# Optimization experiments

Hardware: AMD Instinct MI355X
Metric: run time of the kernel (lower is better)

## Reference

```python
import jax, jax.numpy as jnp
import numpy as np

B, T, C = 8, 512, 512
H, HKV, D = 8, 4, 64
S_MAX = 128
BASE_FREQ = 10000.0
INIT_SIGMA = 256.0
EPS = 1e-6


def _init_positional_kernel(n_heads, head_dim, s_max, base_freq):
    table_size = 2 * s_max + 1
    deltas = jnp.arange(table_size) - s_max
    d_half = head_dim // 2
    freqs = 1.0 / base_freq ** (jnp.arange(d_half, dtype=jnp.float32) / d_half)
    phases = deltas[:, None].astype(jnp.float32) * freqs[None, :]
    P_single = jnp.concatenate([jnp.cos(phases), jnp.sin(phases)], axis=-1)
    return jnp.tile(P_single[None, :, :], (n_heads, 1, 1))


def setup_inputs() -> dict:
    key = jax.random.key(0)
    ks = jax.random.split(key, 6)
    scale = 0.02
    x = jax.random.normal(ks[0], (B, T, C), dtype=jnp.float32)
    Wq = jax.random.normal(ks[1], (C, H * D), dtype=jnp.float32) * scale
    Wk = jax.random.normal(ks[2], (C, HKV * D), dtype=jnp.float32) * scale
    Wv = jax.random.normal(ks[3], (C, HKV * D), dtype=jnp.float32) * scale
    Wproj = jax.random.normal(ks[4], (C, C), dtype=jnp.float32) * scale
    P = _init_positional_kernel(H, D, S_MAX, BASE_FREQ)
    sigma = jnp.full((H,), INIT_SIGMA, dtype=jnp.float32)
    return {"x": x, "Wq": Wq, "Wk": Wk, "Wv": Wv, "Wproj": Wproj, "P": P, "sigma": sigma}


def _norm(t):
    # nGPT-style: unit norm * sqrt(dim)
    dim = t.shape[-1]
    return t * (jnp.sqrt(float(dim)) * jax.lax.rsqrt((t * t).sum(axis=-1, keepdims=True) + EPS))


def _warped_kernel(P, sigma, T_):
    # P: [H, 2*S_MAX+1, D], sigma: [H] -> P_interp: [H, T, T, D]
    positions = jnp.arange(T_)
    delta = positions[:, None] - positions[None, :]  # [T, T]
    s = jnp.abs(sigma) + 1e-6
    delta_warped = S_MAX * jnp.tanh(delta[None, :, :].astype(jnp.float32) / s[:, None, None])
    delta_table = delta_warped + S_MAX  # [H, T, T]
    idx_lo = jnp.floor(delta_table).astype(jnp.int32)
    idx_hi = idx_lo + 1
    frac = delta_table - idx_lo.astype(P.dtype)
    table_max = 2 * S_MAX
    idx_lo = jnp.clip(idx_lo, 0, table_max)
    idx_hi = jnp.clip(idx_hi, 0, table_max)
    head_idx = jnp.arange(H)[:, None, None]
    P_lo = P[head_idx, idx_lo, :]  # [H, T, T, D]
    P_hi = P[head_idx, idx_hi, :]
    return (1 - frac[..., None]) * P_lo + frac[..., None] * P_hi


def reference(x, Wq, Wk, Wv, Wproj, P, sigma):
    q = (x @ Wq).reshape(B, T, H, D)
    k = (x @ Wk).reshape(B, T, HKV, D)
    v = (x @ Wv).reshape(B, T, HKV, D)
    q, k = _norm(q), _norm(k)
    repeats = H // HKV
    k = jnp.repeat(k, repeats, axis=2)
    v = jnp.repeat(v, repeats, axis=2)
    q = q.transpose(0, 2, 1, 3)  # [B, H, T, D]
    k = k.transpose(0, 2, 1, 3)
    v = v.transpose(0, 2, 1, 3)

    sm_scale = 1.0 / jnp.sqrt(float(D))
    P_interp = _warped_kernel(P, sigma, T)  # [H, T, T, D]
    S = jnp.einsum('bhid,hijd,bhjd->bhij', q, P_interp, k) * sm_scale
    causal_mask = jnp.tril(jnp.ones((T, T), dtype=jnp.bool_))
    S = jnp.where(causal_mask[None, None, :, :], S, jnp.finfo(S.dtype).min)
    A = jax.nn.softmax(S, axis=-1)
    y = A @ v  # [B, H, T, D]
    y = y.transpose(0, 2, 1, 3).reshape(B, T, H * D)
    return y @ Wproj
```

## Files before the change

kernel.cpp:

```cpp
#include <hip/hip_runtime.h>
#include <hip/hip_bf16.h>
#include <math.h>

#define Bb 8
#define Tt 512
#define Cc 512
#define Hh 8
#define HKV 4
#define Dd 64

typedef __attribute__((ext_vector_type(8))) short short8;
typedef __attribute__((ext_vector_type(4))) float float4v;
typedef __attribute__((ext_vector_type(2))) __fp16 h2;

__device__ __forceinline__ h2 u2h(unsigned u) {
  union { unsigned u; h2 h; } x; x.u = u; return x.h;
}
__device__ __forceinline__ unsigned h2u(h2 h) {
  union { h2 h; unsigned u; } x; x.h = h; return x.u;
}
__device__ __forceinline__ float fdot2(h2 a, h2 b, float c) {
#if __has_builtin(__builtin_amdgcn_fdot2)
  return __builtin_amdgcn_fdot2(a, b, c, false);
#else
  return fmaf((float)a.x, (float)b.x, fmaf((float)a.y, (float)b.y, c));
#endif
}

__device__ __forceinline__ float wave_reduce_sum(float v) {
#pragma unroll
  for (int off = 32; off > 0; off >>= 1) v += __shfl_xor(v, off, 64);
  return v;
}
__device__ __forceinline__ unsigned pack_bf2(float a, float b) {
  __hip_bfloat162 h = __float22bfloat162_rn(make_float2(a, b));
  return *(unsigned*)&h;
}

__global__ __launch_bounds__(256) void prep(
    const float* __restrict__ x, const float* __restrict__ Wq,
    const float* __restrict__ Wk, const float* __restrict__ Wv,
    const float* __restrict__ Wp, const float* __restrict__ P,
    const float* __restrict__ sigma,
    unsigned short* __restrict__ xb, unsigned short* __restrict__ Wtq,
    unsigned short* __restrict__ Wtp, unsigned short* __restrict__ Pwh) {
  const int bid = blockIdx.x;
  const int t = threadIdx.x;
  if (bid < 1024) {
    int i = (bid * 256 + t) * 8;
    float4 f0 = *(const float4*)&x[i];
    float4 f1 = *(const float4*)&x[i + 4];
    unsigned u[4] = {pack_bf2(f0.x, f0.y), pack_bf2(f0.z, f0.w),
                     pack_bf2(f1.x, f1.y), pack_bf2(f1.z, f1.w)};
    *(uint4*)&xb[i] = *(uint4*)u;
  } else if (bid < 1216) {
    __shared__ float Ts[64][65];
    const int bx = bid - 1024;
    const int k0 = (bx & 7) << 6;
    const int n0 = (bx >> 3) << 6;
    const float* src; int ld, nc0; unsigned short* dst; int ndst;
    if (n0 < 512)       { src = Wq; ld = 512; nc0 = n0;        dst = Wtq; ndst = n0; }
    else if (n0 < 768)  { src = Wk; ld = 256; nc0 = n0 - 512;  dst = Wtq; ndst = n0; }
    else if (n0 < 1024) { src = Wv; ld = 256; nc0 = n0 - 768;  dst = Wtq; ndst = n0; }
    else                { src = Wp; ld = 512; nc0 = n0 - 1024; dst = Wtp; ndst = n0 - 1024; }
    const int r = t >> 4, c4 = (t & 15) << 2;
#pragma unroll
    for (int rr = 0; rr < 4; ++rr) {
      int row = (rr << 4) + r;
      float4 f = *(const float4*)&src[(k0 + row) * ld + nc0 + c4];
      Ts[row][c4] = f.x; Ts[row][c4 + 1] = f.y;
      Ts[row][c4 + 2] = f.z; Ts[row][c4 + 3] = f.w;
    }
    __syncthreads();
#pragma unroll
    for (int rr = 0; rr < 4; ++rr) {
      int nr = (rr << 4) + r;
      unsigned u0 = pack_bf2(Ts[c4][nr], Ts[c4 + 1][nr]);
      unsigned u1 = pack_bf2(Ts[c4 + 2][nr], Ts[c4 + 3][nr]);
      *(uint2*)&dst[(ndst + nr) * 512 + k0 + c4] = make_uint2(u0, u1);
    }
  } else {
    int idx = (bid - 1216) * 256 + t;
    int d = idx & 63;
    int rem = idx >> 6;
    int dd = rem % 1023;
    int h = rem / 1023;
    float s = fabsf(sigma[h]) + 1e-6f;
    float delta = (float)(dd - 511);
    float dt = 128.0f * tanhf(delta / s) + 128.0f;
    float lo = floorf(dt);
    int ilo = (int)lo;
    float frac = dt - lo;
    ilo = max(0, min(ilo, 256));
    int ihi = min(ilo + 1, 256);
    const float* Pb = P + h * 257 * 64;
    float val = (1.0f - frac) * Pb[ilo * 64 + d] + frac * Pb[ihi * 64 + d];
    __fp16 hv = (__fp16)val;
    Pwh[idx] = *(unsigned short*)&hv;
  }
}

__global__ __launch_bounds__(256) void qkv_mfma(
    const unsigned short* __restrict__ xb, const unsigned short* __restrict__ Wt,
    unsigned short* __restrict__ qh, unsigned short* __restrict__ kh,
    unsigned* __restrict__ vhu) {
  __shared__ unsigned short As[64][72];
  __shared__ unsigned short Bs[64][72];
  const int m0 = blockIdx.x * 64;
  const int n0 = blockIdx.y * 64;
  const int t = threadIdx.x;
  const int w = t >> 6, lane = t & 63;
  const int srow = t >> 2, sc = (t & 3) << 4;
  float4v acc[4] = {{0,0,0,0},{0,0,0,0},{0,0,0,0},{0,0,0,0}};
  for (int k0 = 0; k0 < 512; k0 += 64) {
    uint4 a0 = *(const uint4*)&xb[(m0 + srow) * 512 + k0 + sc];
    uint4 a1 = *(const uint4*)&xb[(m0 + srow) * 512 + k0 + sc + 8];
    uint4 b0 = *(const uint4*)&Wt[(n0 + srow) * 512 + k0 + sc];
    uint4 b1 = *(const uint4*)&Wt[(n0 + srow) * 512 + k0 + sc + 8];
    __syncthreads();
    *(uint4*)&As[srow][sc] = a0; *(uint4*)&As[srow][sc + 8] = a1;
    *(uint4*)&Bs[srow][sc] = b0; *(uint4*)&Bs[srow][sc + 8] = b1;
    __syncthreads();
    const int ml = (w << 4) + (lane & 15);
    const int kq = (lane >> 4) << 3;
    short8 aF0 = *(short8*)&As[ml][kq];
    short8 aF1 = *(short8*)&As[ml][kq + 32];
#pragma unroll
    for (int nt = 0; nt < 4; ++nt) {
      const int nl = (nt << 4) + (lane & 15);
      short8 bF0 = *(short8*)&Bs[nl][kq];
      short8 bF1 = *(short8*)&Bs[nl][kq + 32];
      acc[nt] = __builtin_amdgcn_mfma_f32_16x16x32_bf16(aF0, bF0, acc[nt], 0, 0, 0);
      acc[nt] = __builtin_amdgcn_mfma_f32_16x16x32_bf16(aF1, bF1, acc[nt], 0, 0, 0);
    }
  }
  const int lane15 = lane & 15;
  const int rowbase = m0 + (w << 4) + ((lane >> 4) << 2);
  if (n0 < 768) {
#pragma unroll
    for (int r = 0; r < 4; ++r) {
      float ss = 0.0f;
#pragma unroll
      for (int nt = 0; nt < 4; ++nt) ss = fmaf(acc[nt][r], acc[nt][r], ss);
#pragma unroll
      for (int off = 1; off < 16; off <<= 1) ss += __shfl_xor(ss, off, 64);
      float sc2 = 8.0f * rsqrtf(ss + 1e-6f);
      const int row = rowbase + r;
      if (n0 < 512) {
        const int h = n0 >> 6;
#pragma unroll
        for (int nt = 0; nt < 4; ++nt) {
          __fp16 hv = (__fp16)(acc[nt][r] * sc2);
          qh[(row * Hh + h) * Dd + (nt << 4) + lane15] = *(unsigned short*)&hv;
        }
      } else {
        const int hkv = (n0 - 512) >> 6;
#pragma unroll
        for (int nt = 0; nt < 4; ++nt) {
          __fp16 hv = (__fp16)(acc[nt][r] * sc2);
          kh[(row * HKV + hkv) * Dd + (nt << 4) + lane15] = *(unsigned short*)&hv;
        }
      }
    }
  } else {
    const int hkv = (n0 - 768) >> 6;
#pragma unroll
    for (int r = 0; r < 4; r += 2) {
      const int rp = (rowbase + r) >> 1;
#pragma unroll
      for (int nt = 0; nt < 4; ++nt) {
        unsigned u = h2u(__builtin_amdgcn_cvt_pkrtz(acc[nt][r], acc[nt][r + 1]));
        vhu[(rp * HKV + hkv) * Dd + (nt << 4) + lane15] = u;
      }
    }
  }
}

__global__ __launch_bounds__(256) void proj_mfma(
    const unsigned short* __restrict__ yb, const unsigned short* __restrict__ Wt,
    float* __restrict__ out) {
  __shared__ unsigned short As[64][72];
  __shared__ unsigned short Bs[64][72];
  const int m0 = blockIdx.x * 64;
  const int n0 = blockIdx.y * 64;
  const int t = threadIdx.x;
  const int w = t >> 6, lane = t & 63;
  const int srow = t >> 2, sc = (t & 3) << 4;
  float4v acc[4] = {{0,0,0,0},{0,0,0,0},{0,0,0,0},{0,0,0,0}};
  for (int k0 = 0; k0 < 512; k0 += 64) {
    uint4 a0 = *(const uint4*)&yb[(m0 + srow) * 512 + k0 + sc];
    uint4 a1 = *(const uint4*)&yb[(m0 + srow) * 512 + k0 + sc + 8];
    uint4 b0 = *(const uint4*)&Wt[(n0 + srow) * 512 + k0 + sc];
    uint4 b1 = *(const uint4*)&Wt[(n0 + srow) * 512 + k0 + sc + 8];
    __syncthreads();
    *(uint4*)&As[srow][sc] = a0; *(uint4*)&As[srow][sc + 8] = a1;
    *(uint4*)&Bs[srow][sc] = b0; *(uint4*)&Bs[srow][sc + 8] = b1;
    __syncthreads();
    const int ml = (w << 4) + (lane & 15);
    const int kq = (lane >> 4) << 3;
    short8 aF0 = *(short8*)&As[ml][kq];
    short8 aF1 = *(short8*)&As[ml][kq + 32];
#pragma unroll
    for (int nt = 0; nt < 4; ++nt) {
      const int nl = (nt << 4) + (lane & 15);
      short8 bF0 = *(short8*)&Bs[nl][kq];
      short8 bF1 = *(short8*)&Bs[nl][kq + 32];
      acc[nt] = __builtin_amdgcn_mfma_f32_16x16x32_bf16(aF0, bF0, acc[nt], 0, 0, 0);
      acc[nt] = __builtin_amdgcn_mfma_f32_16x16x32_bf16(aF1, bF1, acc[nt], 0, 0, 0);
    }
  }
#pragma unroll
  for (int nt = 0; nt < 4; ++nt) {
    int col = n0 + (nt << 4) + (lane & 15);
#pragma unroll
    for (int r = 0; r < 4; ++r) {
      int row = m0 + (w << 4) + ((lane >> 4) << 2) + r;
      out[row * 512 + col] = acc[nt][r];
    }
  }
}

__global__ __launch_bounds__(256) void attn(
    const unsigned short* __restrict__ qh, const unsigned short* __restrict__ kh,
    const unsigned* __restrict__ vhu, const unsigned short* __restrict__ Pwh,
    unsigned short* __restrict__ yb) {
  __shared__ __fp16 PwS[96][72];
  __shared__ __fp16 pS[4][32][16];

  const int t = threadIdx.x;
  const int lane = t & 63;
  const int wu = __builtin_amdgcn_readfirstlane(t >> 6);
  const int bh = blockIdx.x;
  const int b = bh >> 3;
  const int h = bh & 7;
  const int hkv = h >> 1;
  const int i0 = 480 - blockIdx.y * 32;

  float l_lane[8], o_run[8];
#pragma unroll
  for (int r = 0; r < 8; ++r) { l_lane[r] = 0.0f; o_run[r] = 0.0f; }

  const int prow = (wu << 3) + 63 - lane;
  const int i_base = i0 + (wu << 3);
  const unsigned short* qbase = &qh[((b * Tt + i_base) * Hh + h) * Dd];

  for (int jt0 = 0; jt0 <= i0 + 31; jt0 += 64) {
    __syncthreads();
    {
      int jr = t >> 2, dc = (t & 3) << 4;
      const int pb0 = h * 1023 + (i0 - jt0) + 448;
      const unsigned short* pwp = &Pwh[(pb0 + jr) * 64 + dc];
      *(uint4*)&PwS[jr][dc]     = *(const uint4*)&pwp[0];
      *(uint4*)&PwS[jr][dc + 8] = *(const uint4*)&pwp[8];
      int pr2 = 64 + (t >> 3), dc2 = (t & 7) << 3;
      if (pr2 < 95)
        *(uint4*)&PwS[pr2][dc2] = *(const uint4*)&Pwh[(pb0 + pr2) * 64 + dc2];
    }
    uint4 kr[8];
    {
      const uint4* kp = (const uint4*)&kh[((b * Tt + jt0 + lane) * HKV + hkv) * Dd];
#pragma unroll
      for (int c = 0; c < 8; ++c) kr[c] = kp[c];
    }
    __syncthreads();

    const int j = jt0 + lane;
    float pv8[8];
#pragma unroll
    for (int r = 0; r < 8; ++r) {
      const uint4* qp = (const uint4*)&qbase[r * (Hh * Dd)];
      float sr = 0.0f;
#pragma unroll
      for (int ch = 0; ch < 8; ++ch) {
        uint4 qu = qp[ch];
        uint4 pu = *(uint4*)&PwS[prow + r][ch << 3];
        sr = fdot2(u2h(qu.x) * u2h(pu.x), u2h(kr[ch].x), sr);
        sr = fdot2(u2h(qu.y) * u2h(pu.y), u2h(kr[ch].y), sr);
        sr = fdot2(u2h(qu.z) * u2h(pu.z), u2h(kr[ch].z), sr);
        sr = fdot2(u2h(qu.w) * u2h(pu.w), u2h(kr[ch].w), sr);
      }
      float sv = (j <= i_base + r) ? sr * 0.125f : -1e30f;
      float p = __expf(sv - 6.0f);
      l_lane[r] += p;
      pv8[r] = p;
    }
    {
      unsigned u[8];
#pragma unroll
      for (int r = 0; r < 8; ++r) {
        float other = __shfl_xor(pv8[r], 1, 64);
        u[r] = h2u(__builtin_amdgcn_cvt_pkrtz(pv8[r], other));
      }
      if (!(lane & 1)) {
        *(uint4*)&pS[wu][lane >> 1][0] = *(uint4*)&u[0];
        *(uint4*)&pS[wu][lane >> 1][8] = *(uint4*)&u[4];
      }
    }

    const unsigned* vp = &vhu[(((b * Tt + jt0) >> 1) * HKV + hkv) * Dd + lane];
#pragma unroll 4
    for (int j2 = 0; j2 < 32; ++j2) {
      uint4 p0 = *(uint4*)&pS[wu][j2][0];
      uint4 p1 = *(uint4*)&pS[wu][j2][8];
      h2 vv = u2h(vp[j2 * (HKV * Dd)]);
      o_run[0] = fdot2(u2h(p0.x), vv, o_run[0]);
      o_run[1] = fdot2(u2h(p0.y), vv, o_run[1]);
      o_run[2] = fdot2(u2h(p0.z), vv, o_run[2]);
      o_run[3] = fdot2(u2h(p0.w), vv, o_run[3]);
      o_run[4] = fdot2(u2h(p1.x), vv, o_run[4]);
      o_run[5] = fdot2(u2h(p1.y), vv, o_run[5]);
      o_run[6] = fdot2(u2h(p1.z), vv, o_run[6]);
      o_run[7] = fdot2(u2h(p1.w), vv, o_run[7]);
    }
  }
#pragma unroll
  for (int r = 0; r < 8; ++r) {
    float l = wave_reduce_sum(l_lane[r]);
    const int i_r = i_base + r;
    __hip_bfloat16 hv = __float2bfloat16(o_run[r] / l);
    yb[((b * Tt + i_r) * Hh + h) * Dd + lane] = *(unsigned short*)&hv;
  }
}

extern "C" void kernel_launch(void* const* d_in, const int* in_sizes, int n_in,
                              void* d_out, int out_size, void* d_ws, size_t ws_size,
                              hipStream_t stream) {
  const float* x     = (const float*)d_in[0];
  const float* Wq    = (const float*)d_in[1];
  const float* Wk    = (const float*)d_in[2];
  const float* Wv    = (const float*)d_in[3];
  const float* Wproj = (const float*)d_in[4];
  const float* P     = (const float*)d_in[5];
  const float* sigma = (const float*)d_in[6];
  float* out = (float*)d_out;

  float* ws = (float*)d_ws;
  unsigned short* qh  = (unsigned short*)ws;
  unsigned short* kh  = (unsigned short*)(ws + 1048576);
  unsigned*       vhu = (unsigned*)(ws + 1572864);
  unsigned short* Pwh = (unsigned short*)(ws + 2097152);
  unsigned short* xb  = (unsigned short*)(ws + 2359296);
  unsigned short* yb  = xb;
  unsigned short* Wtq = (unsigned short*)(ws + 3407872);
  unsigned short* Wtp = (unsigned short*)(ws + 3670016);

  prep<<<dim3(3262), 256, 0, stream>>>(x, Wq, Wk, Wv, Wproj, P, sigma,
                                       xb, Wtq, Wtp, Pwh);
  qkv_mfma<<<dim3(64, 16), 256, 0, stream>>>(xb, Wtq, qh, kh, vhu);
  attn<<<dim3(64, 16), 256, 0, stream>>>(qh, kh, vhu, Pwh, yb);
  proj_mfma<<<dim3(64, 8), 256, 0, stream>>>(yb, Wtp, out);
}
```

Before: 146.8 us.

## Use MFMA for P·V in attention with transposed V layout

The P·V product in the attention kernel now runs on 16x16x32 f16 MFMA instructions instead of per-lane fdot2 loops. To feed it, the QKV kernel writes V transposed per batch and KV head (d-major, t contiguous). Probabilities go to a shared 32x64 tile and the row sums are reduced through shared memory before the final normalisation. This adds an extra block-wide barrier per key tile and changes the output store pattern, in exchange for cutting the scalar dot-product work for the value accumulation.

```diff
diff --git a/kernel.cpp b/kernel.cpp
--- a/kernel.cpp
+++ b/kernel.cpp
@@ -12,6 +12,7 @@
 typedef __attribute__((ext_vector_type(8))) short short8;
 typedef __attribute__((ext_vector_type(4))) float float4v;
 typedef __attribute__((ext_vector_type(2))) __fp16 h2;
+typedef __attribute__((ext_vector_type(8))) __fp16 half8;
 
 __device__ __forceinline__ h2 u2h(unsigned u) {
   union { unsigned u; h2 h; } x; x.u = u; return x.h;
@@ -103,7 +104,7 @@
 __global__ __launch_bounds__(256) void qkv_mfma(
     const unsigned short* __restrict__ xb, const unsigned short* __restrict__ Wt,
     unsigned short* __restrict__ qh, unsigned short* __restrict__ kh,
-    unsigned* __restrict__ vhu) {
+    unsigned short* __restrict__ vT) {
   __shared__ unsigned short As[64][72];
   __shared__ unsigned short Bs[64][72];
   const int m0 = blockIdx.x * 64;
@@ -164,14 +165,14 @@
     }
   } else {
     const int hkv = (n0 - 768) >> 6;
-#pragma unroll
-    for (int r = 0; r < 4; r += 2) {
-      const int rp = (rowbase + r) >> 1;
-#pragma unroll
-      for (int nt = 0; nt < 4; ++nt) {
-        unsigned u = h2u(__builtin_amdgcn_cvt_pkrtz(acc[nt][r], acc[nt][r + 1]));
-        vhu[(rp * HKV + hkv) * Dd + (nt << 4) + lane15] = u;
-      }
+    const int bb = rowbase >> 9;
+    const int trow = rowbase & 511;
+#pragma unroll
+    for (int nt = 0; nt < 4; ++nt) {
+      const int d = (nt << 4) + lane15;
+      unsigned u0 = h2u(__builtin_amdgcn_cvt_pkrtz(acc[nt][0], acc[nt][1]));
+      unsigned u1 = h2u(__builtin_amdgcn_cvt_pkrtz(acc[nt][2], acc[nt][3]));
+      *(uint2*)&vT[((bb * HKV + hkv) * 64 + d) * 512 + trow] = make_uint2(u0, u1);
     }
   }
 }
@@ -222,10 +223,11 @@
 
 __global__ __launch_bounds__(256) void attn(
     const unsigned short* __restrict__ qh, const unsigned short* __restrict__ kh,
-    const unsigned* __restrict__ vhu, const unsigned short* __restrict__ Pwh,
+    const unsigned short* __restrict__ vT, const unsigned short* __restrict__ Pwh,
     unsigned short* __restrict__ yb) {
   __shared__ __fp16 PwS[96][72];
-  __shared__ __fp16 pS[4][32][16];
+  __shared__ __fp16 pS[32][72];
+  __shared__ float lS[32];
 
   const int t = threadIdx.x;
   const int lane = t & 63;
@@ -236,13 +238,20 @@
   const int hkv = h >> 1;
   const int i0 = 480 - blockIdx.y * 32;
 
-  float l_lane[8], o_run[8];
-#pragma unroll
-  for (int r = 0; r < 8; ++r) { l_lane[r] = 0.0f; o_run[r] = 0.0f; }
+  float l_lane[8];
+#pragma unroll
+  for (int r = 0; r < 8; ++r) l_lane[r] = 0.0f;
+  float4v oacc[2] = {{0, 0, 0, 0}, {0, 0, 0, 0}};
 
   const int prow = (wu << 3) + 63 - lane;
   const int i_base = i0 + (wu << 3);
   const unsigned short* qbase = &qh[((b * Tt + i_base) * Hh + h) * Dd];
+
+  const int i16 = (wu & 1) << 4;
+  const int dt0 = (wu >> 1) << 1;
+  const int lm = lane & 15;
+  const int kq = (lane >> 4) << 3;
+  const unsigned short* vTbase = &vT[((b * HKV + hkv) * 64) * 512];
 
   for (int jt0 = 0; jt0 <= i0 + 31; jt0 += 64) {
     __syncthreads();
@@ -265,7 +274,6 @@
     __syncthreads();
 
     const int j = jt0 + lane;
-    float pv8[8];
 #pragma unroll
     for (int r = 0; r < 8; ++r) {
       const uint4* qp = (const uint4*)&qbase[r * (Hh * Dd)];
@@ -282,43 +290,39 @@
       float sv = (j <= i_base + r) ? sr * 0.125f : -1e30f;
       float p = __expf(sv - 6.0f);
       l_lane[r] += p;
-      pv8[r] = p;
-    }
-    {
-      unsigned u[8];
-#pragma unroll
-      for (int r = 0; r < 8; ++r) {
-        float other = __shfl_xor(pv8[r], 1, 64);
-        u[r] = h2u(__builtin_amdgcn_cvt_pkrtz(pv8[r], other));
-      }
-      if (!(lane & 1)) {
-        *(uint4*)&pS[wu][lane >> 1][0] = *(uint4*)&u[0];
-        *(uint4*)&pS[wu][lane >> 1][8] = *(uint4*)&u[4];
-      }
-    }
-
-    const unsigned* vp = &vhu[(((b * Tt + jt0) >> 1) * HKV + hkv) * Dd + lane];
-#pragma unroll 4
-    for (int j2 = 0; j2 < 32; ++j2) {
-      uint4 p0 = *(uint4*)&pS[wu][j2][0];
-      uint4 p1 = *(uint4*)&pS[wu][j2][8];
-      h2 vv = u2h(vp[j2 * (HKV * Dd)]);
-      o_run[0] = fdot2(u2h(p0.x), vv, o_run[0]);
-      o_run[1] = fdot2(u2h(p0.y), vv, o_run[1]);
-      o_run[2] = fdot2(u2h(p0.z), vv, o_run[2]);
-      o_run[3] = fdot2(u2h(p0.w), vv, o_run[3]);
-      o_run[4] = fdot2(u2h(p1.x), vv, o_run[4]);
-      o_run[5] = fdot2(u2h(p1.y), vv, o_run[5]);
-      o_run[6] = fdot2(u2h(p1.z), vv, o_run[6]);
-      o_run[7] = fdot2(u2h(p1.w), vv, o_run[7]);
-    }
-  }
+      pS[(wu << 3) + r][lane] = (__fp16)p;
+    }
+    __syncthreads();
+
+    half8 a0 = *(half8*)&pS[i16 + lm][kq];
+    half8 a1 = *(half8*)&pS[i16 + lm][kq + 32];
+#pragma unroll
+    for (int dd = 0; dd < 2; ++dd) {
+      const unsigned short* vp = vTbase + (((dt0 + dd) << 4) + lm) * 512 + jt0 + kq;
+      half8 b0 = *(const half8*)&vp[0];
+      half8 b1 = *(const half8*)&vp[32];
+      oacc[dd] = __builtin_amdgcn_mfma_f32_16x16x32_f16(a0, b0, oacc[dd], 0, 0, 0);
+      oacc[dd] = __builtin_amdgcn_mfma_f32_16x16x32_f16(a1, b1, oacc[dd], 0, 0, 0);
+    }
+  }
+
 #pragma unroll
   for (int r = 0; r < 8; ++r) {
-    float l = wave_reduce_sum(l_lane[r]);
-    const int i_r = i_base + r;
-    __hip_bfloat16 hv = __float2bfloat16(o_run[r] / l);
-    yb[((b * Tt + i_r) * Hh + h) * Dd + lane] = *(unsigned short*)&hv;
+    float lr = wave_reduce_sum(l_lane[r]);
+    if (lane == r) lS[(wu << 3) + r] = lr;
+  }
+  __syncthreads();
+
+#pragma unroll
+  for (int dd = 0; dd < 2; ++dd) {
+    const int d = ((dt0 + dd) << 4) + lm;
+#pragma unroll
+    for (int r = 0; r < 4; ++r) {
+      const int irow = i16 + ((lane >> 4) << 2) + r;
+      const float val = oacc[dd][r] / lS[irow];
+      __hip_bfloat16 hv = __float2bfloat16(val);
+      yb[((b * Tt + i0 + irow) * Hh + h) * Dd + d] = *(unsigned short*)&hv;
+    }
   }
 }
 
@@ -337,7 +341,7 @@
   float* ws = (float*)d_ws;
   unsigned short* qh  = (unsigned short*)ws;
   unsigned short* kh  = (unsigned short*)(ws + 1048576);
-  unsigned*       vhu = (unsigned*)(ws + 1572864);
+  unsigned short* vT  = (unsigned short*)(ws + 1572864);
   unsigned short* Pwh = (unsigned short*)(ws + 2097152);
   unsigned short* xb  = (unsigned short*)(ws + 2359296);
   unsigned short* yb  = xb;
@@ -346,7 +350,7 @@
 
   prep<<<dim3(3262), 256, 0, stream>>>(x, Wq, Wk, Wv, Wproj, P, sigma,
                                        xb, Wtq, Wtp, Pwh);
-  qkv_mfma<<<dim3(64, 16), 256, 0, stream>>>(xb, Wtq, qh, kh, vhu);
-  attn<<<dim3(64, 16), 256, 0, stream>>>(qh, kh, vhu, Pwh, yb);
+  qkv_mfma<<<dim3(64, 16), 256, 0, stream>>>(xb, Wtq, qh, kh, vT);
+  attn<<<dim3(64, 16), 256, 0, stream>>>(qh, kh, vT, Pwh, yb);
   proj_mfma<<<dim3(64, 8), 256, 0, stream>>>(yb, Wtp, out);
 }
```

After: 136.8 us. -6.8%, faster.
